# Kernel optimization log

Hardware: AMD Instinct MI355X
Metric: run time of the kernel (lower is better)

## Reference

```python
import jax, jax.numpy as jnp
import numpy as np

NE, NPER = 100000, 50000        # empresa / persona node counts
D_EMP, D_PER = 64, 32           # raw feature dims
H, OUT = 128, 64                # hidden_channels, out_channels
E_EE, E_PE, E_EP = 1600000, 800000, 800000
NEG_SLOPE = 0.2                 # GATConv leaky_relu slope


def setup_inputs() -> dict:
    key = jax.random.key(0)
    ks = jax.random.split(key, 40)

    def w(k, fi, fo):
        return jax.random.normal(k, (fi, fo), jnp.float32) / jnp.sqrt(jnp.float32(fi))

    def b(k, n):
        return jax.random.normal(k, (n,), jnp.float32) * 0.02

    return {
        "x_emp": jax.random.normal(ks[0], (NE, D_EMP), jnp.float32),
        "x_per": jax.random.normal(ks[1], (NPER, D_PER), jnp.float32),
        "ee_src": jax.random.randint(ks[2], (E_EE,), 0, NE, jnp.int32),
        "ee_dst": jax.random.randint(ks[3], (E_EE,), 0, NE, jnp.int32),
        "pe_src": jax.random.randint(ks[4], (E_PE,), 0, NPER, jnp.int32),
        "pe_dst": jax.random.randint(ks[5], (E_PE,), 0, NE, jnp.int32),
        "ep_src": jax.random.randint(ks[6], (E_EP,), 0, NE, jnp.int32),
        "ep_dst": jax.random.randint(ks[7], (E_EP,), 0, NPER, jnp.int32),
        # per-node-type input projections
        "lin_emp_w": w(ks[8], D_EMP, H), "lin_emp_b": b(ks[9], H),
        "lin_per_w": w(ks[10], D_PER, H), "lin_per_b": b(ks[11], H),
        # conv1: SAGEConv per edge type (H -> H)
        "s1_ee_Wl": w(ks[12], H, H), "s1_ee_bl": b(ks[13], H), "s1_ee_Wr": w(ks[14], H, H),
        "s1_pe_Wl": w(ks[15], H, H), "s1_pe_bl": b(ks[16], H), "s1_pe_Wr": w(ks[17], H, H),
        "s1_ep_Wl": w(ks[18], H, H), "s1_ep_bl": b(ks[19], H), "s1_ep_Wr": w(ks[20], H, H),
        # conv2: GATConv on empresa->empresa (H -> OUT, heads=1)
        "gat_Wsrc": w(ks[21], H, OUT), "gat_Wdst": w(ks[22], H, OUT),
        "gat_asrc": b(ks[23], OUT), "gat_adst": b(ks[24], OUT), "gat_b": b(ks[25], OUT),
        # conv2: SAGEConv on remaining edge types (H -> OUT)
        "s2_pe_Wl": w(ks[26], H, OUT), "s2_pe_bl": b(ks[27], OUT), "s2_pe_Wr": w(ks[28], H, OUT),
        "s2_ep_Wl": w(ks[29], H, OUT), "s2_ep_bl": b(ks[30], OUT), "s2_ep_Wr": w(ks[31], H, OUT),
    }


def _sage(h_src, h_dst, src, dst, Wl, bl, Wr, n_dst):
    # SAGEConv: mean-aggregate neighbor features, then lin_l(agg) + lin_r(x_dst)
    agg = jax.ops.segment_sum(h_src[src], dst, num_segments=n_dst)
    cnt = jax.ops.segment_sum(jnp.ones((src.shape[0], 1), h_src.dtype), dst,
                              num_segments=n_dst)
    mean = agg / jnp.maximum(cnt, 1.0)  # isolated nodes -> 0 (PyG mean behavior)
    return mean @ Wl + bl + h_dst @ Wr


def _gat(h, src, dst, Wsrc, Wdst, asrc, adst, bias, n):
    # GATConv, heads=1, no self loops: edge-softmax attention over dst neighborhoods
    zs = h @ Wsrc                                   # [n, OUT]
    zd = h @ Wdst
    e = (zs @ asrc)[src] + (zd @ adst)[dst]         # [E] attention logits
    e = jnp.where(e > 0, e, NEG_SLOPE * e)          # leaky_relu(0.2)
    m = jax.ops.segment_max(e, dst, num_segments=n)
    ex = jnp.exp(e - m[dst])
    den = jax.ops.segment_sum(ex, dst, num_segments=n)
    alpha = ex / den[dst]                           # softmax per dst node
    out = jax.ops.segment_sum(zs[src] * alpha[:, None], dst, num_segments=n)
    return out + bias


def reference(x_emp, x_per, ee_src, ee_dst, pe_src, pe_dst, ep_src, ep_dst,
              lin_emp_w, lin_emp_b, lin_per_w, lin_per_b,
              s1_ee_Wl, s1_ee_bl, s1_ee_Wr,
              s1_pe_Wl, s1_pe_bl, s1_pe_Wr,
              s1_ep_Wl, s1_ep_bl, s1_ep_Wr,
              gat_Wsrc, gat_Wdst, gat_asrc, gat_adst, gat_b,
              s2_pe_Wl, s2_pe_bl, s2_pe_Wr,
              s2_ep_Wl, s2_ep_bl, s2_ep_Wr):
    # per-node-type input Linear + relu
    h_emp = jax.nn.relu(x_emp @ lin_emp_w + lin_emp_b)
    h_per = jax.nn.relu(x_per @ lin_per_w + lin_per_b)

    # conv1: HeteroConv of SAGEConvs, aggr='sum' across relations per dst type
    emp1 = (_sage(h_emp, h_emp, ee_src, ee_dst, s1_ee_Wl, s1_ee_bl, s1_ee_Wr, NE)
            + _sage(h_per, h_emp, pe_src, pe_dst, s1_pe_Wl, s1_pe_bl, s1_pe_Wr, NE))
    per1 = _sage(h_emp, h_per, ep_src, ep_dst, s1_ep_Wl, s1_ep_bl, s1_ep_Wr, NPER)
    emp1 = jax.nn.relu(emp1)
    per1 = jax.nn.relu(per1)

    # conv2: GAT on empresa->empresa, SAGE elsewhere, sum across relations
    emp2 = (_gat(emp1, ee_src, ee_dst, gat_Wsrc, gat_Wdst, gat_asrc, gat_adst, gat_b, NE)
            + _sage(per1, emp1, pe_src, pe_dst, s2_pe_Wl, s2_pe_bl, s2_pe_Wr, NE))
    per2 = _sage(emp1, per1, ep_src, ep_dst, s2_ep_Wl, s2_ep_bl, s2_ep_Wr, NPER)
    return emp2, per2
```

## Files before the change

kernel.cpp:

```cpp
#include <hip/hip_runtime.h>
#include <cstdint>

#define NE_N   100000
#define NPER_N 50000
#define HD     128
#define OUTD   64
#define NEE    1600000
#define NPE    800000
#define NEP    800000
#define ETOT   (NEE+NPE+NEP)

static inline int ceil_div(long long a, long long b){ return (int)((a + b - 1)/b); }

__device__ __forceinline__ float4 ld4(const float* p){ return *reinterpret_cast<const float4*>(p); }
__device__ __forceinline__ void st4(float* p, float4 v){ *reinterpret_cast<float4*>(p) = v; }
__device__ __forceinline__ uint16_t f2b(float f){
    uint32_t u = __float_as_uint(f);
    u += 0x7fffu + ((u >> 16) & 1u);
    return (uint16_t)(u >> 16);
}
__device__ __forceinline__ float b2f(uint32_t u){ return __uint_as_float(u << 16); }

typedef short v8s __attribute__((ext_vector_type(8)));
typedef float v4f __attribute__((ext_vector_type(4)));
typedef float v4fl __attribute__((ext_vector_type(4)));

struct Seg { const uint16_t* W; const float* b; void* C; int ldw; int ldc; int mode; };
struct Segs { Seg s[6]; };

template<int K>
__global__ __launch_bounds__(256)
void gemm_mfma(const uint16_t* __restrict__ A, int N, Segs segs)
{
    constexpr int NKS  = K / 32;
    constexpr int PADK = K + 8;
    __shared__ __align__(16) uint16_t Wt[64 * PADK];

    Seg sg = segs.s[blockIdx.y];

    const int t = threadIdx.x;
    for (int i = t; i < K*64; i += 256){
        int k = i >> 6, c = i & 63;
        Wt[c*PADK + k] = sg.W[(size_t)k*sg.ldw + c];
    }
    __syncthreads();

    const int lane = t & 63, wid = t >> 6;
    const int l16 = lane & 15, lg = lane >> 4;
    const int rowbase = blockIdx.x*256 + wid*64;

    v4f acc[4][4];
#pragma unroll
    for (int i=0;i<4;i++)
#pragma unroll
        for (int j=0;j<4;j++) acc[i][j] = (v4f){0.f,0.f,0.f,0.f};

#pragma unroll
    for (int ks=0; ks<NKS; ks++){
        const int koff = ks*32 + lg*8;
        v8s a[4], b[4];
#pragma unroll
        for (int rt=0;rt<4;rt++){
            int r = rowbase + rt*16 + l16; if (r > N-1) r = N-1;
            a[rt] = *reinterpret_cast<const v8s*>(&A[(size_t)r*K + koff]);
        }
#pragma unroll
        for (int ct=0;ct<4;ct++)
            b[ct] = *reinterpret_cast<const v8s*>(&Wt[(ct*16 + l16)*PADK + koff]);
#pragma unroll
        for (int rt=0;rt<4;rt++)
#pragma unroll
            for (int ct=0;ct<4;ct++)
                acc[rt][ct] = __builtin_amdgcn_mfma_f32_16x16x32_bf16(a[rt], b[ct], acc[rt][ct], 0, 0, 0);
    }

    const int mode = sg.mode, ldc = sg.ldc;
    float bias[4];
    if (mode != 1){
#pragma unroll
        for (int ct=0;ct<4;ct++) bias[ct] = sg.b[ct*16 + l16];
    }
#pragma unroll
    for (int rt=0;rt<4;rt++){
#pragma unroll
        for (int rg=0;rg<4;rg++){
            int r = rowbase + rt*16 + lg*4 + rg;
            if (r < N){
#pragma unroll
                for (int ct=0;ct<4;ct++){
                    float v = acc[rt][ct][rg];
                    int c = ct*16 + l16;
                    if (mode == 0)
                        ((float*)sg.C)[(size_t)r*ldc + c] = v + bias[ct];
                    else if (mode == 1)
                        ((uint16_t*)sg.C)[(size_t)r*ldc + c] = f2b(v);
                    else if (mode == 2)
                        ((uint16_t*)sg.C)[(size_t)r*ldc + c] = f2b(fmaxf(v + bias[ct], 0.f));
                    else
                        ((uint16_t*)sg.C)[(size_t)r*ldc + c] = f2b(v + bias[ct]);
                }
            }
        }
    }
}

__global__ void count_sharded(const int* __restrict__ ee, const int* __restrict__ pe,
                              const int* __restrict__ ep, int* __restrict__ cnt){
    int r = blockIdx.x & 7;
    int i = (blockIdx.x >> 3)*256 + threadIdx.x;
    int d, base, n;
    if (i < NEE){ d = __builtin_nontemporal_load(&ee[i]); base = 0; n = NE_N; }
    else if (i < NEE+NPE){ d = __builtin_nontemporal_load(&pe[i-NEE]); base = 100000; n = NE_N; }
    else if (i < ETOT){ d = __builtin_nontemporal_load(&ep[i-NEE-NPE]); base = 200000; n = NPER_N; }
    else return;
    int seg = n >> 3;
    if (d >= r*seg && d < (r+1)*seg) atomicAdd(&cnt[base + d], 1);
}
__global__ __launch_bounds__(256)
void scan_block3(const int* __restrict__ cnt_all, int* __restrict__ ee_off,
                 int* __restrict__ pe_off, int* __restrict__ ep_off,
                 int* __restrict__ partial){
    int r = blockIdx.y;
    const int* cnt = cnt_all + (r==0 ? 0 : (r==1 ? 100000 : 200000));
    int* off = (r==0) ? ee_off : (r==1 ? pe_off : ep_off);
    int n = (r==2) ? NPER_N : NE_N;
    int* part = partial + r*128;

    __shared__ int sh[256];
    int t = threadIdx.x;
    int base = blockIdx.x*1024 + t*4;
    int v0 = (base  <n)?cnt[base  ]:0;
    int v1 = (base+1<n)?cnt[base+1]:0;
    int v2 = (base+2<n)?cnt[base+2]:0;
    int v3 = (base+3<n)?cnt[base+3]:0;
    int tsum = v0+v1+v2+v3;
    sh[t]=tsum; __syncthreads();
    for (int d=1; d<256; d<<=1){
        int x = (t>=d)? sh[t-d] : 0;
        __syncthreads();
        sh[t] += x;
        __syncthreads();
    }
    int ex = sh[t]-tsum;
    if (base  <n) off[base  ]=ex;
    if (base+1<n) off[base+1]=ex+v0;
    if (base+2<n) off[base+2]=ex+v0+v1;
    if (base+3<n) off[base+3]=ex+v0+v1+v2;
    if (t==255) part[blockIdx.x]=sh[255];
}
__global__ void scan_partial3(int* __restrict__ partial){
    int r = blockIdx.x;
    if (threadIdx.x != 0) return;
    int n = (r==2) ? NPER_N : NE_N;
    int nb = (n + 1023) >> 10;
    int* p = partial + r*128;
    int run = 0;
    for (int i=0;i<nb;i++){ int v=p[i]; p[i]=run; run+=v; }
}
__global__ void add_base3(int* __restrict__ ee_off, int* __restrict__ pe_off,
                          int* __restrict__ ep_off, const int* __restrict__ partial){
    int i = blockIdx.x*blockDim.x + threadIdx.x;
    if (i <= NE_N){
        if (i < NE_N) ee_off[i] += partial[i>>10];
        else ee_off[NE_N] = NEE;
    } else if (i <= 2*NE_N + 1){
        int k = i - (NE_N+1);
        if (k < NE_N) pe_off[k] += partial[128 + (k>>10)];
        else pe_off[NE_N] = NPE;
    } else {
        int k = i - 2*(NE_N+1);
        if (k < NPER_N) ep_off[k] += partial[256 + (k>>10)];
        else if (k == NPER_N) ep_off[NPER_N] = NEP;
    }
}
__global__ void fill_sharded(const int* __restrict__ ee_src, const int* __restrict__ ee_dst,
                             const int* __restrict__ pe_src, const int* __restrict__ pe_dst,
                             const int* __restrict__ ep_src, const int* __restrict__ ep_dst,
                             const int* __restrict__ ee_off, const int* __restrict__ pe_off,
                             const int* __restrict__ ep_off, int* __restrict__ cnt_all,
                             int* __restrict__ ee_csr, int* __restrict__ pe_csr,
                             int* __restrict__ ep_csr){
    int r = blockIdx.x & 7;
    int i = (blockIdx.x >> 3)*256 + threadIdx.x;
    int d, base, n;
    const int* srcp; const int* offp; int* csrp;
    if (i < NEE){ d = __builtin_nontemporal_load(&ee_dst[i]); base = 0; n = NE_N; srcp = ee_src; offp = ee_off; csrp = ee_csr; }
    else if (i < NEE+NPE){ i -= NEE; d = __builtin_nontemporal_load(&pe_dst[i]); base = 100000; n = NE_N; srcp = pe_src; offp = pe_off; csrp = pe_csr; }
    else if (i < ETOT){ i -= NEE+NPE; d = __builtin_nontemporal_load(&ep_dst[i]); base = 200000; n = NPER_N; srcp = ep_src; offp = ep_off; csrp = ep_csr; }
    else return;
    int seg = n >> 3;
    if (d >= r*seg && d < (r+1)*seg){
        int old = atomicAdd(&cnt_all[base + d], -1);
        csrp[offp[d] + old - 1] = __builtin_nontemporal_load(&srcp[i]);
    }
}

__global__ __launch_bounds__(256)
void agg_emp1(const uint16_t* __restrict__ proj_ee, const uint16_t* __restrict__ proj_pe,
              const int* __restrict__ ee_off, const int* __restrict__ ee_csr,
              const int* __restrict__ pe_off, const int* __restrict__ pe_csr,
              uint16_t* __restrict__ emp1b){
    int w    = (blockIdx.x*blockDim.x + threadIdx.x) >> 6;
    int lane = threadIdx.x & 63;
    if (w >= NE_N) return;
    int grp = lane >> 4, l16 = lane & 15;

    float a[8] = {0,0,0,0,0,0,0,0};
    int b = ee_off[w], e = ee_off[w+1];
    int dee = e - b;
    for (int cb=b; cb<e; cb+=64){
        int j = cb + lane;
        int s = (j<e) ? ee_csr[j] : -1;
        int lim = e - cb; if (lim > 64) lim = 64;
        int iters = (lim + 3) >> 2;
        for (int k=0;k<iters;k++){
            int sg = __shfl(s, k*4 + grp, 64);
            if (sg >= 0){
                uint4 u = *reinterpret_cast<const uint4*>(&proj_ee[(size_t)sg*128 + l16*8]);
                a[0]+=b2f(u.x&0xffffu); a[1]+=b2f(u.x>>16);
                a[2]+=b2f(u.y&0xffffu); a[3]+=b2f(u.y>>16);
                a[4]+=b2f(u.z&0xffffu); a[5]+=b2f(u.z>>16);
                a[6]+=b2f(u.w&0xffffu); a[7]+=b2f(u.w>>16);
            }
        }
    }
    float c[8] = {0,0,0,0,0,0,0,0};
    b = pe_off[w]; e = pe_off[w+1];
    int dpe = e - b;
    for (int cb=b; cb<e; cb+=64){
        int j = cb + lane;
        int s = (j<e) ? pe_csr[j] : -1;
        int lim = e - cb; if (lim > 64) lim = 64;
        int iters = (lim + 3) >> 2;
        for (int k=0;k<iters;k++){
            int sg = __shfl(s, k*4 + grp, 64);
            if (sg >= 0){
                uint4 u = *reinterpret_cast<const uint4*>(&proj_pe[(size_t)sg*128 + l16*8]);
                c[0]+=b2f(u.x&0xffffu); c[1]+=b2f(u.x>>16);
                c[2]+=b2f(u.y&0xffffu); c[3]+=b2f(u.y>>16);
                c[4]+=b2f(u.z&0xffffu); c[5]+=b2f(u.z>>16);
                c[6]+=b2f(u.w&0xffffu); c[7]+=b2f(u.w>>16);
            }
        }
    }
#pragma unroll
    for (int f=0;f<8;f++){
        a[f] += __shfl_xor(a[f],16,64); a[f] += __shfl_xor(a[f],32,64);
        c[f] += __shfl_xor(c[f],16,64); c[f] += __shfl_xor(c[f],32,64);
    }
    if (grp == 0){
        float s1f = 1.f/fmaxf((float)dee,1.f);
        float s2f = 1.f/fmaxf((float)dpe,1.f);
        uint4 sb = *reinterpret_cast<const uint4*>(&emp1b[(size_t)w*128 + l16*8]);
        float sf[8] = { b2f(sb.x&0xffffu), b2f(sb.x>>16), b2f(sb.y&0xffffu), b2f(sb.y>>16),
                        b2f(sb.z&0xffffu), b2f(sb.z>>16), b2f(sb.w&0xffffu), b2f(sb.w>>16) };
        uint32_t o[8];
#pragma unroll
        for (int f=0;f<8;f++) o[f] = (uint32_t)f2b(fmaxf(sf[f] + a[f]*s1f + c[f]*s2f, 0.f));
        uint4 pk;
        pk.x = o[0] | (o[1]<<16); pk.y = o[2] | (o[3]<<16);
        pk.z = o[4] | (o[5]<<16); pk.w = o[6] | (o[7]<<16);
        *reinterpret_cast<uint4*>(&emp1b[(size_t)w*128 + l16*8]) = pk;
    }
}
__global__ __launch_bounds__(256)
void agg_per1(const uint16_t* __restrict__ proj_ep,
              const int* __restrict__ ep_off, const int* __restrict__ ep_csr,
              uint16_t* __restrict__ per1b){
    int w    = (blockIdx.x*blockDim.x + threadIdx.x) >> 6;
    int lane = threadIdx.x & 63;
    if (w >= NPER_N) return;
    int grp = lane >> 4, l16 = lane & 15;

    float a[8] = {0,0,0,0,0,0,0,0};
    int b = ep_off[w], e = ep_off[w+1];
    int deg = e - b;
    for (int cb=b; cb<e; cb+=64){
        int j = cb + lane;
        int s = (j<e) ? ep_csr[j] : -1;
        int lim = e - cb; if (lim > 64) lim = 64;
        int iters = (lim + 3) >> 2;
        for (int k=0;k<iters;k++){
            int sg = __shfl(s, k*4 + grp, 64);
            if (sg >= 0){
                uint4 u = *reinterpret_cast<const uint4*>(&proj_ep[(size_t)sg*128 + l16*8]);
                a[0]+=b2f(u.x&0xffffu); a[1]+=b2f(u.x>>16);
                a[2]+=b2f(u.y&0xffffu); a[3]+=b2f(u.y>>16);
                a[4]+=b2f(u.z&0xffffu); a[5]+=b2f(u.z>>16);
                a[6]+=b2f(u.w&0xffffu); a[7]+=b2f(u.w>>16);
            }
        }
    }
#pragma unroll
    for (int f=0;f<8;f++){
        a[f] += __shfl_xor(a[f],16,64); a[f] += __shfl_xor(a[f],32,64);
    }
    if (grp == 0){
        float s1f = 1.f/fmaxf((float)deg,1.f);
        uint4 sb = *reinterpret_cast<const uint4*>(&per1b[(size_t)w*128 + l16*8]);
        float sf[8] = { b2f(sb.x&0xffffu), b2f(sb.x>>16), b2f(sb.y&0xffffu), b2f(sb.y>>16),
                        b2f(sb.z&0xffffu), b2f(sb.z>>16), b2f(sb.w&0xffffu), b2f(sb.w>>16) };
        uint32_t o[8];
#pragma unroll
        for (int f=0;f<8;f++) o[f] = (uint32_t)f2b(fmaxf(sf[f] + a[f]*s1f, 0.f));
        uint4 pk;
        pk.x = o[0] | (o[1]<<16); pk.y = o[2] | (o[3]<<16);
        pk.z = o[4] | (o[5]<<16); pk.w = o[6] | (o[7]<<16);
        *reinterpret_cast<uint4*>(&per1b[(size_t)w*128 + l16*8]) = pk;
    }
}
__global__ __launch_bounds__(256)
void agg_per2(const uint16_t* __restrict__ p2ep,
              const int* __restrict__ ep_off, const int* __restrict__ ep_csr,
              float* __restrict__ out){
    int w    = (blockIdx.x*blockDim.x + threadIdx.x) >> 6;
    int lane = threadIdx.x & 63;
    if (w >= NPER_N) return;
    int grp = lane >> 4, l16 = lane & 15;

    float a[4] = {0,0,0,0};
    int b = ep_off[w], e = ep_off[w+1];
    int deg = e - b;
    for (int cb=b; cb<e; cb+=64){
        int j = cb + lane;
        int s = (j<e) ? ep_csr[j] : -1;
        int lim = e - cb; if (lim > 64) lim = 64;
        int iters = (lim + 3) >> 2;
        for (int k=0;k<iters;k++){
            int sg = __shfl(s, k*4 + grp, 64);
            if (sg >= 0){
                uint2 u = *reinterpret_cast<const uint2*>(&p2ep[(size_t)sg*64 + l16*4]);
                a[0]+=b2f(u.x&0xffffu); a[1]+=b2f(u.x>>16);
                a[2]+=b2f(u.y&0xffffu); a[3]+=b2f(u.y>>16);
            }
        }
    }
#pragma unroll
    for (int f=0;f<4;f++){
        a[f] += __shfl_xor(a[f],16,64); a[f] += __shfl_xor(a[f],32,64);
    }
    if (grp == 0){
        float s1f = 1.f/fmaxf((float)deg,1.f);
        float4 o4 = ld4(&out[(size_t)w*64 + l16*4]);
        o4.x += a[0]*s1f; o4.y += a[1]*s1f; o4.z += a[2]*s1f; o4.w += a[3]*s1f;
        st4(&out[(size_t)w*64 + l16*4], o4);
    }
}
__global__ __launch_bounds__(256)
void gat_sage_emp2(const int* __restrict__ ee_off, const int* __restrict__ ee_csr,
                   const int* __restrict__ pe_off, const int* __restrict__ pe_csr,
                   const float* __restrict__ as, const float* __restrict__ ad,
                   const uint16_t* __restrict__ zs, const uint16_t* __restrict__ p2pe,
                   float* __restrict__ out){
    int w    = (blockIdx.x*blockDim.x + threadIdx.x) >> 6;
    int lane = threadIdx.x & 63;
    if (w >= NE_N) return;
    int grp = lane >> 4, l16 = lane & 15;

    float g[4] = {0,0,0,0};
    float invden = 0.f;
    int b = ee_off[w], e = ee_off[w+1];
    if (e > b){
        float add = ad[w];
        float m = -INFINITY;
        for (int j=b+lane; j<e; j+=64){
            float ev = as[ee_csr[j]] + add;
            ev = ev > 0.f ? ev : 0.2f*ev;
            m = fmaxf(m, ev);
        }
        for (int o=32;o;o>>=1) m = fmaxf(m, __shfl_xor(m,o,64));

        float den = 0.f;
        for (int cb=b; cb<e; cb+=64){
            int j = cb + lane;
            int s = 0; float ex = 0.f;
            if (j < e){
                s = ee_csr[j];
                float ev = as[s] + add;
                ev = ev > 0.f ? ev : 0.2f*ev;
                ex = expf(ev - m);
            }
            den += ex;
            int lim = e - cb; if (lim > 64) lim = 64;
            int iters = (lim + 3) >> 2;
            for (int k=0;k<iters;k++){
                int   sg = __shfl(s,  k*4 + grp, 64);
                float ag = __shfl(ex, k*4 + grp, 64);
                uint2 u = *reinterpret_cast<const uint2*>(&zs[(size_t)sg*64 + l16*4]);
                g[0] += ag*b2f(u.x&0xffffu); g[1] += ag*b2f(u.x>>16);
                g[2] += ag*b2f(u.y&0xffffu); g[3] += ag*b2f(u.y>>16);
            }
        }
        for (int o=32;o;o>>=1) den += __shfl_xor(den,o,64);
        invden = 1.f/den;
    }

    float p[4] = {0,0,0,0};
    b = pe_off[w]; e = pe_off[w+1];
    int deg = e - b;
    for (int cb=b; cb<e; cb+=64){
        int j = cb + lane;
        int s = (j<e) ? pe_csr[j] : -1;
        int lim = e - cb; if (lim > 64) lim = 64;
        int iters = (lim + 3) >> 2;
        for (int k=0;k<iters;k++){
            int sg = __shfl(s, k*4 + grp, 64);
            if (sg >= 0){
                uint2 u = *reinterpret_cast<const uint2*>(&p2pe[(size_t)sg*64 + l16*4]);
                p[0]+=b2f(u.x&0xffffu); p[1]+=b2f(u.x>>16);
                p[2]+=b2f(u.y&0xffffu); p[3]+=b2f(u.y>>16);
            }
        }
    }
#pragma unroll
    for (int f=0;f<4;f++){
        g[f] += __shfl_xor(g[f],16,64); g[f] += __shfl_xor(g[f],32,64);
        p[f] += __shfl_xor(p[f],16,64); p[f] += __shfl_xor(p[f],32,64);
    }
    if (grp == 0){
        float s2f = 1.f/fmaxf((float)deg,1.f);
        float4 o4 = ld4(&out[(size_t)w*64 + l16*4]);
        o4.x += g[0]*invden + p[0]*s2f;
        o4.y += g[1]*invden + p[1]*s2f;
        o4.z += g[2]*invden + p[2]*s2f;
        o4.w += g[3]*invden + p[3]*s2f;
        st4(&out[(size_t)w*64 + l16*4], o4);
    }
}

__global__ void rowdots(const uint16_t* __restrict__ ZS, const uint16_t* __restrict__ E1,
                        const float* __restrict__ wa, const float* __restrict__ wv,
                        float* __restrict__ a_s, float* __restrict__ a_d){
    int wid  = (blockIdx.x*blockDim.x + threadIdx.x) >> 6;
    int lane = threadIdx.x & 63;
    if (wid < NE_N){
        float v = b2f((uint32_t)ZS[(size_t)wid*64 + lane])*wa[lane];
        for (int o=32;o;o>>=1) v += __shfl_xor(v,o,64);
        if (lane==0) a_s[wid]=v;
    } else if (wid < 2*NE_N){
        int k = wid - NE_N;
        float v = b2f((uint32_t)E1[(size_t)k*128 + lane])*wv[lane]
                + b2f((uint32_t)E1[(size_t)k*128 + 64 + lane])*wv[64+lane];
        for (int o=32;o;o>>=1) v += __shfl_xor(v,o,64);
        if (lane==0) a_d[k]=v;
    }
}

constexpr int WB_WSUM   = 0;
constexpr int WB_EEWL   = 16384;
constexpr int WB_EPWL   = 32768;
constexpr int WB_PEWL   = 49152;
constexpr int WB_EPWR1  = 65536;
constexpr int WB_LINE   = 81920;
constexpr int WB_LINP   = 90112;
constexpr int WB_GATW   = 94208;
constexpr int WB_S2EPWL = 102400;
constexpr int WB_S2PEWR = 110592;
constexpr int WB_S2PEWL = 118784;
constexpr int WB_S2EPWR = 126976;

__global__ void prep(const float* Wr_ee, const float* Wr_pe,
                     const float* ee_Wl, const float* ep_Wl, const float* pe_Wl, const float* ep_Wr,
                     const float* line_w, const float* linp_w,
                     const float* gatW, const float* s2epWl, const float* s2peWr,
                     const float* s2peWl, const float* s2epWr,
                     const float* bl_ee, const float* bl_pe,
                     const float* s2_pe_bl, const float* gat_b,
                     const float* Wdst, const float* adst,
                     uint16_t* wb, float* bsum1, float* b2sum, float* vvec)
{
    int j = blockIdx.x, t = threadIdx.x;
    if (j == 12){
        if (t < HD){
            bsum1[t] = bl_ee[t] + bl_pe[t];
            float s = 0.f;
            for (int c=0;c<OUTD;c++) s += Wdst[t*OUTD + c]*adst[c];
            vvec[t] = s;
        }
        if (t < OUTD) b2sum[t] = s2_pe_bl[t] + gat_b[t];
        return;
    }
    if (j == 0){
        for (int i=t; i<16384; i+=256) wb[WB_WSUM + i] = f2b(Wr_ee[i] + Wr_pe[i]);
        return;
    }
    const float* src; uint16_t* dst; int n;
    switch(j){
        case 1:  src=ee_Wl;  dst=wb+WB_EEWL;   n=16384; break;
        case 2:  src=ep_Wl;  dst=wb+WB_EPWL;   n=16384; break;
        case 3:  src=pe_Wl;  dst=wb+WB_PEWL;   n=16384; break;
        case 4:  src=ep_Wr;  dst=wb+WB_EPWR1;  n=16384; break;
        case 5:  src=line_w; dst=wb+WB_LINE;   n=8192;  break;
        case 6:  src=linp_w; dst=wb+WB_LINP;   n=4096;  break;
        case 7:  src=gatW;   dst=wb+WB_GATW;   n=8192;  break;
        case 8:  src=s2epWl; dst=wb+WB_S2EPWL; n=8192;  break;
        case 9:  src=s2peWr; dst=wb+WB_S2PEWR; n=8192;  break;
        case 10: src=s2peWl; dst=wb+WB_S2PEWL; n=8192;  break;
        default: src=s2epWr; dst=wb+WB_S2EPWR; n=8192;  break;
    }
    for (int i=t; i<n; i+=256) dst[i] = f2b(src[i]);
}

__global__ void convx(const float* __restrict__ xe, const float* __restrict__ xp,
                      uint16_t* __restrict__ be, uint16_t* __restrict__ bp){
    const int NE4 = NE_N*64/4, NP4 = NPER_N*32/4;
    int i = blockIdx.x*blockDim.x + threadIdx.x;
    if (i < NE4){
        v4fl v = __builtin_nontemporal_load(reinterpret_cast<const v4fl*>(xe + (size_t)i*4));
        uint2 o;
        o.x = (uint32_t)f2b(v.x) | ((uint32_t)f2b(v.y) << 16);
        o.y = (uint32_t)f2b(v.z) | ((uint32_t)f2b(v.w) << 16);
        *reinterpret_cast<uint2*>(&be[(size_t)i*4]) = o;
    } else if (i < NE4 + NP4){
        int k = i - NE4;
        v4fl v = __builtin_nontemporal_load(reinterpret_cast<const v4fl*>(xp + (size_t)k*4));
        uint2 o;
        o.x = (uint32_t)f2b(v.x) | ((uint32_t)f2b(v.y) << 16);
        o.y = (uint32_t)f2b(v.z) | ((uint32_t)f2b(v.w) << 16);
        *reinterpret_cast<uint2*>(&bp[(size_t)k*4]) = o;
    }
}

constexpr size_t OFF_R0 = 0;
constexpr size_t OFF_R1 = 3200000;
constexpr size_t OFF_R2 = 4800000;
constexpr size_t OFF_R3 = 11200000;
constexpr size_t OFF_R4 = 14400000;
constexpr size_t OFF_R5 = 27200000;
constexpr size_t OFF_R6 = 33600000;
constexpr size_t OFF_R7 = 40000000;
constexpr size_t OFF_R8 = 43200000;
constexpr size_t OFF_AS = 49600000;
constexpr size_t OFF_AD = 49700000;
constexpr size_t OFF_WB = 49800000;
constexpr size_t OFF_BS1= 49900000;
constexpr size_t OFF_BS2= 49900128;
constexpr size_t OFF_VV = 49900192;
constexpr size_t OFF_CNT    = 50000000;
constexpr size_t OFF_EE_OFF = 50250000;
constexpr size_t OFF_PE_OFF = 50350008;
constexpr size_t OFF_EP_OFF = 50450016;
constexpr size_t OFF_PART   = 50500024;
constexpr size_t OFF_EE_CSR = 50500416;
constexpr size_t OFF_PE_CSR = 52100416;
constexpr size_t OFF_EP_CSR = 52900416;

extern "C" void kernel_launch(void* const* d_in, const int* in_sizes, int n_in,
                              void* d_out, int out_size, void* d_ws, size_t ws_size,
                              hipStream_t stream)
{
    const float* x_emp = (const float*)d_in[0];
    const float* x_per = (const float*)d_in[1];
    const int* ee_src = (const int*)d_in[2];
    const int* ee_dst = (const int*)d_in[3];
    const int* pe_src = (const int*)d_in[4];
    const int* pe_dst = (const int*)d_in[5];
    const int* ep_src = (const int*)d_in[6];
    const int* ep_dst = (const int*)d_in[7];
    const float* lin_emp_w=(const float*)d_in[8],  *lin_emp_b=(const float*)d_in[9];
    const float* lin_per_w=(const float*)d_in[10], *lin_per_b=(const float*)d_in[11];
    const float* s1_ee_Wl=(const float*)d_in[12], *s1_ee_bl=(const float*)d_in[13], *s1_ee_Wr=(const float*)d_in[14];
    const float* s1_pe_Wl=(const float*)d_in[15], *s1_pe_bl=(const float*)d_in[16], *s1_pe_Wr=(const float*)d_in[17];
    const float* s1_ep_Wl=(const float*)d_in[18], *s1_ep_bl=(const float*)d_in[19], *s1_ep_Wr=(const float*)d_in[20];
    const float* gat_Wsrc=(const float*)d_in[21], *gat_Wdst=(const float*)d_in[22];
    const float* gat_asrc=(const float*)d_in[23], *gat_adst=(const float*)d_in[24], *gat_b=(const float*)d_in[25];
    const float* s2_pe_Wl=(const float*)d_in[26], *s2_pe_bl=(const float*)d_in[27], *s2_pe_Wr=(const float*)d_in[28];
    const float* s2_ep_Wl=(const float*)d_in[29], *s2_ep_bl=(const float*)d_in[30], *s2_ep_Wr=(const float*)d_in[31];

    float* ws = (float*)d_ws;
    int*   wi = (int*)d_ws;
    float* out_emp = (float*)d_out;
    float* out_per = out_emp + (size_t)NE_N*OUTD;

    uint16_t* xbe     = (uint16_t*)(ws + OFF_R0);
    uint16_t* zsB     = (uint16_t*)(ws + OFF_R0);
    uint16_t* xbp     = (uint16_t*)(ws + OFF_R1);
    uint16_t* p2peB   = (uint16_t*)(ws + OFF_R1);
    uint16_t* h_empB  = (uint16_t*)(ws + OFF_R2);
    uint16_t* h_perB  = (uint16_t*)(ws + OFF_R3);
    uint16_t* emp1B   = (uint16_t*)(ws + OFF_R4);
    uint16_t* per1B   = (uint16_t*)(ws + OFF_R4 + 6400000);
    uint16_t* p2epB   = (uint16_t*)(ws + OFF_R5);
    uint16_t* proj_eeB= (uint16_t*)(ws + OFF_R6);
    uint16_t* proj_peB= (uint16_t*)(ws + OFF_R7);
    uint16_t* proj_epB= (uint16_t*)(ws + OFF_R8);
    float* a_s   = ws + OFF_AS;
    float* a_d   = ws + OFF_AD;
    uint16_t* WB = (uint16_t*)(ws + OFF_WB);
    float* bsum1 = ws + OFF_BS1;
    float* b2sum = ws + OFF_BS2;
    float* vvec  = ws + OFF_VV;

    int* cnt_all = wi + OFF_CNT;
    int* ee_off = wi + OFF_EE_OFF; int* ee_csr = wi + OFF_EE_CSR;
    int* pe_off = wi + OFF_PE_OFF; int* pe_csr = wi + OFF_PE_CSR;
    int* ep_off = wi + OFF_EP_OFF; int* ep_csr = wi + OFF_EP_CSR;
    int* part   = wi + OFF_PART;

    const int GE = ceil_div(NE_N,256), GP = ceil_div(NPER_N,256);

    hipMemsetAsync(cnt_all, 0, 250000*sizeof(int), stream);

    prep<<<13,256,0,stream>>>(s1_ee_Wr, s1_pe_Wr, s1_ee_Wl, s1_ep_Wl, s1_pe_Wl, s1_ep_Wr,
                              lin_emp_w, lin_per_w,
                              gat_Wsrc, s2_ep_Wl, s2_pe_Wr, s2_pe_Wl, s2_ep_Wr,
                              s1_ee_bl, s1_pe_bl, s2_pe_bl, gat_b, gat_Wdst, gat_adst,
                              WB, bsum1, b2sum, vvec);
    convx<<<ceil_div(NE_N*64/4 + NPER_N*32/4, 256),256,0,stream>>>(x_emp, x_per, xbe, xbp);

    const int NCHUNK = ceil_div(ETOT,256);
    count_sharded<<<NCHUNK*8,256,0,stream>>>(ee_dst, pe_dst, ep_dst, cnt_all);
    scan_block3<<<dim3(ceil_div(NE_N,1024),3),256,0,stream>>>(cnt_all, ee_off, pe_off, ep_off, part);
    scan_partial3<<<3,64,0,stream>>>(part);
    add_base3<<<ceil_div(2*(NE_N+1)+NPER_N+1,256),256,0,stream>>>(ee_off, pe_off, ep_off, part);
    fill_sharded<<<NCHUNK*8,256,0,stream>>>(ee_src, ee_dst, pe_src, pe_dst, ep_src, ep_dst,
                                            ee_off, pe_off, ep_off, cnt_all,
                                            ee_csr, pe_csr, ep_csr);

    {
        Segs g{};
        g.s[0] = Seg{WB+WB_LINE,    lin_emp_b,    (void*)h_empB,      128,128,2};
        g.s[1] = Seg{WB+WB_LINE+64, lin_emp_b+64, (void*)(h_empB+64), 128,128,2};
        g.s[2]=g.s[0]; g.s[3]=g.s[0]; g.s[4]=g.s[0]; g.s[5]=g.s[0];
        gemm_mfma<64><<<dim3(GE,2),256,0,stream>>>(xbe, NE_N, g);
    }
    {
        Segs g{};
        g.s[0] = Seg{WB+WB_LINP,    lin_per_b,    (void*)h_perB,      128,128,2};
        g.s[1] = Seg{WB+WB_LINP+64, lin_per_b+64, (void*)(h_perB+64), 128,128,2};
        g.s[2]=g.s[0]; g.s[3]=g.s[0]; g.s[4]=g.s[0]; g.s[5]=g.s[0];
        gemm_mfma<32><<<dim3(GP,2),256,0,stream>>>(xbp, NPER_N, g);
    }
    {
        Segs g{};
        g.s[0] = Seg{WB+WB_WSUM,    bsum1,    (void*)emp1B,        128,128,3};
        g.s[1] = Seg{WB+WB_WSUM+64, bsum1+64, (void*)(emp1B+64),   128,128,3};
        g.s[2] = Seg{WB+WB_EEWL,    nullptr,  (void*)proj_eeB,     128,128,1};
        g.s[3] = Seg{WB+WB_EEWL+64, nullptr,  (void*)(proj_eeB+64),128,128,1};
        g.s[4] = Seg{WB+WB_EPWL,    nullptr,  (void*)proj_epB,     128,128,1};
        g.s[5] = Seg{WB+WB_EPWL+64, nullptr,  (void*)(proj_epB+64),128,128,1};
        gemm_mfma<128><<<dim3(GE,6),256,0,stream>>>(h_empB, NE_N, g);
    }
    {
        Segs g{};
        g.s[0] = Seg{WB+WB_PEWL,    nullptr,     (void*)proj_peB,     128,128,1};
        g.s[1] = Seg{WB+WB_PEWL+64, nullptr,     (void*)(proj_peB+64),128,128,1};
        g.s[2] = Seg{WB+WB_EPWR1,   s1_ep_bl,    (void*)per1B,        128,128,3};
        g.s[3] = Seg{WB+WB_EPWR1+64,s1_ep_bl+64, (void*)(per1B+64),   128,128,3};
        g.s[4]=g.s[0]; g.s[5]=g.s[0];
        gemm_mfma<128><<<dim3(GP,4),256,0,stream>>>(h_perB, NPER_N, g);
    }
    agg_emp1<<<ceil_div((long long)NE_N*64,256),256,0,stream>>>(proj_eeB, proj_peB, ee_off, ee_csr, pe_off, pe_csr, emp1B);
    agg_per1<<<ceil_div((long long)NPER_N*64,256),256,0,stream>>>(proj_epB, ep_off, ep_csr, per1B);

    {
        Segs g{};
        g.s[0] = Seg{WB+WB_GATW,   nullptr, (void*)zsB,     64,64,1};
        g.s[1] = Seg{WB+WB_S2EPWL, nullptr, (void*)p2epB,   64,64,1};
        g.s[2] = Seg{WB+WB_S2PEWR, b2sum,   (void*)out_emp, 64,64,0};
        g.s[3]=g.s[0]; g.s[4]=g.s[0]; g.s[5]=g.s[0];
        gemm_mfma<128><<<dim3(GE,3),256,0,stream>>>(emp1B, NE_N, g);
    }
    rowdots<<<ceil_div(2*NE_N,4),256,0,stream>>>(zsB, emp1B, gat_asrc, vvec, a_s, a_d);
    {
        Segs g{};
        g.s[0] = Seg{WB+WB_S2PEWL, nullptr,  (void*)p2peB,   64,64,1};
        g.s[1] = Seg{WB+WB_S2EPWR, s2_ep_bl, (void*)out_per, 64,64,0};
        g.s[2]=g.s[0]; g.s[3]=g.s[0]; g.s[4]=g.s[0]; g.s[5]=g.s[0];
        gemm_mfma<128><<<dim3(GP,2),256,0,stream>>>(per1B, NPER_N, g);
    }

    gat_sage_emp2<<<ceil_div((long long)NE_N*64,256),256,0,stream>>>(ee_off, ee_csr, pe_off, pe_csr, a_s, a_d, zsB, p2peB, out_emp);
    agg_per2<<<ceil_div((long long)NPER_N*64,256),256,0,stream>>>(p2epB, ep_off, ep_csr, out_per);
}
```

Baseline: 797.7 us.

## Fuse GAT attention dots into epilogues, drop max pass, unshard edge count

Computes a_s inside the GEMM epilogue via a new mode that reduces row dots with the source attention vector, and a_d inside the agg_emp1 epilogue, removing the separate rowdots kernel and its re-reads. Removes the per-node max pass in the GAT softmax, computing exp directly. Replaces the 8-way sharded count kernel with a single pass of atomics. Risks exp overflow without max subtraction and more atomic contention in counting.

```diff
diff --git a/kernel.cpp b/kernel.cpp
--- a/kernel.cpp
+++ b/kernel.cpp
@@ -25,7 +25,8 @@
 typedef float v4f __attribute__((ext_vector_type(4)));
 typedef float v4fl __attribute__((ext_vector_type(4)));
 
-struct Seg { const uint16_t* W; const float* b; void* C; int ldw; int ldc; int mode; };
+struct Seg { const uint16_t* W; const float* b; void* C;
+             const float* aux; float* auxout; int ldw; int ldc; int mode; };
 struct Segs { Seg s[6]; };
 
 template<int K>
@@ -76,16 +77,23 @@
 
     const int mode = sg.mode, ldc = sg.ldc;
     float bias[4];
-    if (mode != 1){
+    if (mode == 0 || mode == 2 || mode == 3){
 #pragma unroll
         for (int ct=0;ct<4;ct++) bias[ct] = sg.b[ct*16 + l16];
+    }
+    float aux[4];
+    if (mode == 4){
+#pragma unroll
+        for (int ct=0;ct<4;ct++) aux[ct] = sg.aux[ct*16 + l16];
     }
 #pragma unroll
     for (int rt=0;rt<4;rt++){
 #pragma unroll
         for (int rg=0;rg<4;rg++){
             int r = rowbase + rt*16 + lg*4 + rg;
-            if (r < N){
+            bool valid = (r < N);
+            float partial = 0.f;
+            if (valid){
 #pragma unroll
                 for (int ct=0;ct<4;ct++){
                     float v = acc[rt][ct][rg];
@@ -96,25 +104,31 @@
                         ((uint16_t*)sg.C)[(size_t)r*ldc + c] = f2b(v);
                     else if (mode == 2)
                         ((uint16_t*)sg.C)[(size_t)r*ldc + c] = f2b(fmaxf(v + bias[ct], 0.f));
-                    else
+                    else if (mode == 3)
                         ((uint16_t*)sg.C)[(size_t)r*ldc + c] = f2b(v + bias[ct]);
+                    else {
+                        ((uint16_t*)sg.C)[(size_t)r*ldc + c] = f2b(v);
+                        partial += v*aux[ct];
+                    }
                 }
             }
-        }
-    }
-}
-
-__global__ void count_sharded(const int* __restrict__ ee, const int* __restrict__ pe,
-                              const int* __restrict__ ep, int* __restrict__ cnt){
-    int r = blockIdx.x & 7;
-    int i = (blockIdx.x >> 3)*256 + threadIdx.x;
-    int d, base, n;
-    if (i < NEE){ d = __builtin_nontemporal_load(&ee[i]); base = 0; n = NE_N; }
-    else if (i < NEE+NPE){ d = __builtin_nontemporal_load(&pe[i-NEE]); base = 100000; n = NE_N; }
-    else if (i < ETOT){ d = __builtin_nontemporal_load(&ep[i-NEE-NPE]); base = 200000; n = NPER_N; }
-    else return;
-    int seg = n >> 3;
-    if (d >= r*seg && d < (r+1)*seg) atomicAdd(&cnt[base + d], 1);
+            if (mode == 4){
+                partial += __shfl_xor(partial,1,64);
+                partial += __shfl_xor(partial,2,64);
+                partial += __shfl_xor(partial,4,64);
+                partial += __shfl_xor(partial,8,64);
+                if (valid && l16 == 0) sg.auxout[r] = partial;
+            }
+        }
+    }
+}
+
+__global__ void count_all(const int* __restrict__ ee, const int* __restrict__ pe,
+                          const int* __restrict__ ep, int* __restrict__ cnt){
+    int i = blockIdx.x*blockDim.x + threadIdx.x;
+    if (i < NEE) atomicAdd(&cnt[__builtin_nontemporal_load(&ee[i])], 1);
+    else if (i < NEE+NPE) atomicAdd(&cnt[100000 + __builtin_nontemporal_load(&pe[i-NEE])], 1);
+    else if (i < ETOT) atomicAdd(&cnt[200000 + __builtin_nontemporal_load(&ep[i-NEE-NPE])], 1);
 }
 __global__ __launch_bounds__(256)
 void scan_block3(const int* __restrict__ cnt_all, int* __restrict__ ee_off,
@@ -199,7 +213,8 @@
 void agg_emp1(const uint16_t* __restrict__ proj_ee, const uint16_t* __restrict__ proj_pe,
               const int* __restrict__ ee_off, const int* __restrict__ ee_csr,
               const int* __restrict__ pe_off, const int* __restrict__ pe_csr,
-              uint16_t* __restrict__ emp1b){
+              uint16_t* __restrict__ emp1b,
+              const float* __restrict__ vvec, float* __restrict__ a_d){
     int w    = (blockIdx.x*blockDim.x + threadIdx.x) >> 6;
     int lane = threadIdx.x & 63;
     if (w >= NE_N) return;
@@ -254,13 +269,24 @@
         uint4 sb = *reinterpret_cast<const uint4*>(&emp1b[(size_t)w*128 + l16*8]);
         float sf[8] = { b2f(sb.x&0xffffu), b2f(sb.x>>16), b2f(sb.y&0xffffu), b2f(sb.y>>16),
                         b2f(sb.z&0xffffu), b2f(sb.z>>16), b2f(sb.w&0xffffu), b2f(sb.w>>16) };
-        uint32_t o[8];
-#pragma unroll
-        for (int f=0;f<8;f++) o[f] = (uint32_t)f2b(fmaxf(sf[f] + a[f]*s1f + c[f]*s2f, 0.f));
+        float o[8];
+        float partial = 0.f;
+        uint32_t ob[8];
+#pragma unroll
+        for (int f=0;f<8;f++){
+            o[f] = fmaxf(sf[f] + a[f]*s1f + c[f]*s2f, 0.f);
+            partial += o[f]*vvec[l16*8 + f];
+            ob[f] = (uint32_t)f2b(o[f]);
+        }
         uint4 pk;
-        pk.x = o[0] | (o[1]<<16); pk.y = o[2] | (o[3]<<16);
-        pk.z = o[4] | (o[5]<<16); pk.w = o[6] | (o[7]<<16);
+        pk.x = ob[0] | (ob[1]<<16); pk.y = ob[2] | (ob[3]<<16);
+        pk.z = ob[4] | (ob[5]<<16); pk.w = ob[6] | (ob[7]<<16);
         *reinterpret_cast<uint4*>(&emp1b[(size_t)w*128 + l16*8]) = pk;
+        partial += __shfl_xor(partial,1,64);
+        partial += __shfl_xor(partial,2,64);
+        partial += __shfl_xor(partial,4,64);
+        partial += __shfl_xor(partial,8,64);
+        if (l16 == 0) a_d[w] = partial;
     }
 }
 __global__ __launch_bounds__(256)
@@ -362,14 +388,6 @@
     int b = ee_off[w], e = ee_off[w+1];
     if (e > b){
         float add = ad[w];
-        float m = -INFINITY;
-        for (int j=b+lane; j<e; j+=64){
-            float ev = as[ee_csr[j]] + add;
-            ev = ev > 0.f ? ev : 0.2f*ev;
-            m = fmaxf(m, ev);
-        }
-        for (int o=32;o;o>>=1) m = fmaxf(m, __shfl_xor(m,o,64));
-
         float den = 0.f;
         for (int cb=b; cb<e; cb+=64){
             int j = cb + lane;
@@ -378,7 +396,7 @@
                 s = ee_csr[j];
                 float ev = as[s] + add;
                 ev = ev > 0.f ? ev : 0.2f*ev;
-                ex = expf(ev - m);
+                ex = expf(ev);
             }
             den += ex;
             int lim = e - cb; if (lim > 64) lim = 64;
@@ -425,24 +443,6 @@
         o4.z += g[2]*invden + p[2]*s2f;
         o4.w += g[3]*invden + p[3]*s2f;
         st4(&out[(size_t)w*64 + l16*4], o4);
-    }
-}
-
-__global__ void rowdots(const uint16_t* __restrict__ ZS, const uint16_t* __restrict__ E1,
-                        const float* __restrict__ wa, const float* __restrict__ wv,
-                        float* __restrict__ a_s, float* __restrict__ a_d){
-    int wid  = (blockIdx.x*blockDim.x + threadIdx.x) >> 6;
-    int lane = threadIdx.x & 63;
-    if (wid < NE_N){
-        float v = b2f((uint32_t)ZS[(size_t)wid*64 + lane])*wa[lane];
-        for (int o=32;o;o>>=1) v += __shfl_xor(v,o,64);
-        if (lane==0) a_s[wid]=v;
-    } else if (wid < 2*NE_N){
-        int k = wid - NE_N;
-        float v = b2f((uint32_t)E1[(size_t)k*128 + lane])*wv[lane]
-                + b2f((uint32_t)E1[(size_t)k*128 + 64 + lane])*wv[64+lane];
-        for (int o=32;o;o>>=1) v += __shfl_xor(v,o,64);
-        if (lane==0) a_d[k]=v;
     }
 }
 
@@ -608,64 +608,63 @@
                               WB, bsum1, b2sum, vvec);
     convx<<<ceil_div(NE_N*64/4 + NPER_N*32/4, 256),256,0,stream>>>(x_emp, x_per, xbe, xbp);
 
-    const int NCHUNK = ceil_div(ETOT,256);
-    count_sharded<<<NCHUNK*8,256,0,stream>>>(ee_dst, pe_dst, ep_dst, cnt_all);
+    count_all<<<ceil_div(ETOT,256),256,0,stream>>>(ee_dst, pe_dst, ep_dst, cnt_all);
     scan_block3<<<dim3(ceil_div(NE_N,1024),3),256,0,stream>>>(cnt_all, ee_off, pe_off, ep_off, part);
     scan_partial3<<<3,64,0,stream>>>(part);
     add_base3<<<ceil_div(2*(NE_N+1)+NPER_N+1,256),256,0,stream>>>(ee_off, pe_off, ep_off, part);
+    const int NCHUNK = ceil_div(ETOT,256);
     fill_sharded<<<NCHUNK*8,256,0,stream>>>(ee_src, ee_dst, pe_src, pe_dst, ep_src, ep_dst,
                                             ee_off, pe_off, ep_off, cnt_all,
                                             ee_csr, pe_csr, ep_csr);
 
     {
         Segs g{};
-        g.s[0] = Seg{WB+WB_LINE,    lin_emp_b,    (void*)h_empB,      128,128,2};
-        g.s[1] = Seg{WB+WB_LINE+64, lin_emp_b+64, (void*)(h_empB+64), 128,128,2};
+        g.s[0] = Seg{WB+WB_LINE,    lin_emp_b,    (void*)h_empB,      nullptr,nullptr, 128,128,2};
+        g.s[1] = Seg{WB+WB_LINE+64, lin_emp_b+64, (void*)(h_empB+64), nullptr,nullptr, 128,128,2};
         g.s[2]=g.s[0]; g.s[3]=g.s[0]; g.s[4]=g.s[0]; g.s[5]=g.s[0];
         gemm_mfma<64><<<dim3(GE,2),256,0,stream>>>(xbe, NE_N, g);
     }
     {
         Segs g{};
-        g.s[0] = Seg{WB+WB_LINP,    lin_per_b,    (void*)h_perB,      128,128,2};
-        g.s[1] = Seg{WB+WB_LINP+64, lin_per_b+64, (void*)(h_perB+64), 128,128,2};
+        g.s[0] = Seg{WB+WB_LINP,    lin_per_b,    (void*)h_perB,      nullptr,nullptr, 128,128,2};
+        g.s[1] = Seg{WB+WB_LINP+64, lin_per_b+64, (void*)(h_perB+64), nullptr,nullptr, 128,128,2};
         g.s[2]=g.s[0]; g.s[3]=g.s[0]; g.s[4]=g.s[0]; g.s[5]=g.s[0];
         gemm_mfma<32><<<dim3(GP,2),256,0,stream>>>(xbp, NPER_N, g);
     }
     {
         Segs g{};
-        g.s[0] = Seg{WB+WB_WSUM,    bsum1,    (void*)emp1B,        128,128,3};
-        g.s[1] = Seg{WB+WB_WSUM+64, bsum1+64, (void*)(emp1B+64),   128,128,3};
-        g.s[2] = Seg{WB+WB_EEWL,    nullptr,  (void*)proj_eeB,     128,128,1};
-        g.s[3] = Seg{WB+WB_EEWL+64, nullptr,  (void*)(proj_eeB+64),128,128,1};
-        g.s[4] = Seg{WB+WB_EPWL,    nullptr,  (void*)proj_epB,     128,128,1};
-        g.s[5] = Seg{WB+WB_EPWL+64, nullptr,  (void*)(proj_epB+64),128,128,1};
+        g.s[0] = Seg{WB+WB_WSUM,    bsum1,    (void*)emp1B,        nullptr,nullptr, 128,128,3};
+        g.s[1] = Seg{WB+WB_WSUM+64, bsum1+64, (void*)(emp1B+64),   nullptr,nullptr, 128,128,3};
+        g.s[2] = Seg{WB+WB_EEWL,    nullptr,  (void*)proj_eeB,     nullptr,nullptr, 128,128,1};
+        g.s[3] = Seg{WB+WB_EEWL+64, nullptr,  (void*)(proj_eeB+64),nullptr,nullptr, 128,128,1};
+        g.s[4] = Seg{WB+WB_EPWL,    nullptr,  (void*)proj_epB,     nullptr,nullptr, 128,128,1};
+        g.s[5] = Seg{WB+WB_EPWL+64, nullptr,  (void*)(proj_epB+64),nullptr,nullptr, 128,128,1};
         gemm_mfma<128><<<dim3(GE,6),256,0,stream>>>(h_empB, NE_N, g);
     }
     {
         Segs g{};
-        g.s[0] = Seg{WB+WB_PEWL,    nullptr,     (void*)proj_peB,     128,128,1};
-        g.s[1] = Seg{WB+WB_PEWL+64, nullptr,     (void*)(proj_peB+64),128,128,1};
-        g.s[2] = Seg{WB+WB_EPWR1,   s1_ep_bl,    (void*)per1B,        128,128,3};
-        g.s[3] = Seg{WB+WB_EPWR1+64,s1_ep_bl+64, (void*)(per1B+64),   128,128,3};
+        g.s[0] = Seg{WB+WB_PEWL,    nullptr,     (void*)proj_peB,     nullptr,nullptr, 128,128,1};
+        g.s[1] = Seg{WB+WB_PEWL+64, nullptr,     (void*)(proj_peB+64),nullptr,nullptr, 128,128,1};
+        g.s[2] = Seg{WB+WB_EPWR1,   s1_ep_bl,    (void*)per1B,        nullptr,nullptr, 128,128,3};
+        g.s[3] = Seg{WB+WB_EPWR1+64,s1_ep_bl+64, (void*)(per1B+64),   nullptr,nullptr, 128,128,3};
         g.s[4]=g.s[0]; g.s[5]=g.s[0];
         gemm_mfma<128><<<dim3(GP,4),256,0,stream>>>(h_perB, NPER_N, g);
     }
-    agg_emp1<<<ceil_div((long long)NE_N*64,256),256,0,stream>>>(proj_eeB, proj_peB, ee_off, ee_csr, pe_off, pe_csr, emp1B);
+    agg_emp1<<<ceil_div((long long)NE_N*64,256),256,0,stream>>>(proj_eeB, proj_peB, ee_off, ee_csr, pe_off, pe_csr, emp1B, vvec, a_d);
     agg_per1<<<ceil_div((long long)NPER_N*64,256),256,0,stream>>>(proj_epB, ep_off, ep_csr, per1B);
 
     {
         Segs g{};
-        g.s[0] = Seg{WB+WB_GATW,   nullptr, (void*)zsB,     64,64,1};
-        g.s[1] = Seg{WB+WB_S2EPWL, nullptr, (void*)p2epB,   64,64,1};
-        g.s[2] = Seg{WB+WB_S2PEWR, b2sum,   (void*)out_emp, 64,64,0};
-        g.s[3]=g.s[0]; g.s[4]=g.s[0]; g.s[5]=g.s[0];
+        g.s[0] = Seg{WB+WB_GATW,   nullptr, (void*)zsB,     gat_asrc, a_s,  64,64,4};
+        g.s[1] = Seg{WB+WB_S2EPWL, nullptr, (void*)p2epB,   nullptr, nullptr, 64,64,1};
+        g.s[2] = Seg{WB+WB_S2PEWR, b2sum,   (void*)out_emp, nullptr, nullptr, 64,64,0};
+        g.s[3]=g.s[1]; g.s[4]=g.s[1]; g.s[5]=g.s[1];
         gemm_mfma<128><<<dim3(GE,3),256,0,stream>>>(emp1B, NE_N, g);
     }
-    rowdots<<<ceil_div(2*NE_N,4),256,0,stream>>>(zsB, emp1B, gat_asrc, vvec, a_s, a_d);
     {
         Segs g{};
-        g.s[0] = Seg{WB+WB_S2PEWL, nullptr,  (void*)p2peB,   64,64,1};
-        g.s[1] = Seg{WB+WB_S2EPWR, s2_ep_bl, (void*)out_per, 64,64,0};
+        g.s[0] = Seg{WB+WB_S2PEWL, nullptr,  (void*)p2peB,   nullptr,nullptr, 64,64,1};
+        g.s[1] = Seg{WB+WB_S2EPWR, s2_ep_bl, (void*)out_per, nullptr,nullptr, 64,64,0};
         g.s[2]=g.s[0]; g.s[3]=g.s[0]; g.s[4]=g.s[0]; g.s[5]=g.s[0];
         gemm_mfma<128><<<dim3(GP,2),256,0,stream>>>(per1B, NPER_N, g);
     }
```

Result: faster. 747.1 us (-6.3%).
